# Kernel optimization log

Measured on AMD Instinct MI355X. Metric: run time of the kernel, lower is better.

The kernel has to match this reference:

```python
import jax, jax.numpy as jnp
import numpy as np

N_NODES = 50000
N_EDGES = 800000
NODE_DIM = 128
HIDDEN = 128
N_LAYERS = 2
EPS = 1e-5


def _layer_norm(h, gamma, beta):
    mu = jnp.mean(h, axis=-1, keepdims=True)
    var = jnp.mean(jnp.square(h - mu), axis=-1, keepdims=True)
    return (h - mu) * jax.lax.rsqrt(var + EPS) * gamma + beta


def setup_inputs() -> dict:
    key = jax.random.key(0)
    ks = jax.random.split(key, 12)
    s = 0.05  # small init scale for numerical sanity
    x = jax.random.normal(ks[0], (N_NODES, NODE_DIM), jnp.float32)
    edge_index = jax.random.randint(ks[1], (2, N_EDGES), 0, N_NODES, dtype=jnp.int64)
    # node_encoder: Linear(node_dim -> hidden)
    W_enc = jax.random.normal(ks[2], (HIDDEN, NODE_DIM), jnp.float32) * s
    b_enc = jnp.zeros((HIDDEN,), jnp.float32)
    # per-layer params, stacked over layers (L leading dim)
    Wm1 = jax.random.normal(ks[3], (N_LAYERS, HIDDEN, 2 * HIDDEN), jnp.float32) * s
    bm1 = jnp.zeros((N_LAYERS, HIDDEN), jnp.float32)
    Wm2 = jax.random.normal(ks[4], (N_LAYERS, HIDDEN, HIDDEN), jnp.float32) * s
    bm2 = jnp.zeros((N_LAYERS, HIDDEN), jnp.float32)
    Wu = jax.random.normal(ks[5], (N_LAYERS, HIDDEN, 2 * HIDDEN), jnp.float32) * s
    bu = jnp.zeros((N_LAYERS, HIDDEN), jnp.float32)
    gamma = jnp.ones((N_LAYERS, HIDDEN), jnp.float32)
    beta = jnp.zeros((N_LAYERS, HIDDEN), jnp.float32)
    # output_proj: Linear(hidden -> hidden)
    W_out = jax.random.normal(ks[6], (HIDDEN, HIDDEN), jnp.float32) * s
    b_out = jnp.zeros((HIDDEN,), jnp.float32)
    return {
        "x": x, "edge_index": edge_index,
        "W_enc": W_enc, "b_enc": b_enc,
        "Wm1": Wm1, "bm1": bm1, "Wm2": Wm2, "bm2": bm2,
        "Wu": Wu, "bu": bu, "gamma": gamma, "beta": beta,
        "W_out": W_out, "b_out": b_out,
    }


def reference(x, edge_index, W_enc, b_enc, Wm1, bm1, Wm2, bm2, Wu, bu, gamma, beta, W_out, b_out):
    row, col = edge_index[0], edge_index[1]
    h = x @ W_enc.T + b_enc  # [N, H]
    for l in range(N_LAYERS):
        # gather -> concat -> message MLP  ([E, 2H] -> [E, H])
        m = jnp.concatenate([h[row], h[col]], axis=-1)
        m = jax.nn.relu(m @ Wm1[l].T + bm1[l])
        m = m @ Wm2[l].T + bm2[l]
        # scatter_add over destination nodes (col)
        agg = jax.ops.segment_sum(m, col, num_segments=N_NODES)  # [N, H]
        upd = jnp.concatenate([h, agg], axis=-1) @ Wu[l].T + bu[l]
        h = _layer_norm(h + upd, gamma[l], beta[l])
    return h @ W_out.T + b_out  # node_embeddings [N, H]
```

## Files before the change

kernel.cpp:

```cpp
#include <hip/hip_runtime.h>

#define N_NODES 50000
#define N_EDGES 800000
#define HID 128
#define EPS 1e-5f
#define NBKT 782
#define ESLICE 3125
#define NSLICE 256

typedef __attribute__((ext_vector_type(8))) short s16x8;
typedef __attribute__((ext_vector_type(4))) float f32x4;
typedef __attribute__((ext_vector_type(4))) int i32x4;

__device__ __forceinline__ unsigned short f2bf(float f) {
  unsigned int u = __float_as_uint(f);
  u += 0x7fffu + ((u >> 16) & 1u);
  return (unsigned short)(u >> 16);
}
__device__ __forceinline__ unsigned int pack2(float a, float b) {
  return (unsigned int)f2bf(a) | ((unsigned int)f2bf(b) << 16);
}
__device__ __forceinline__ float bflo(unsigned int u) { return __uint_as_float(u << 16); }
__device__ __forceinline__ float bfhi(unsigned int u) { return __uint_as_float(u & 0xffff0000u); }
__device__ __forceinline__ float bf2f(unsigned short u) { return __uint_as_float((unsigned int)u << 16); }

__global__ __launch_bounds__(256) void prep_hist_kernel(
    const float* __restrict__ W_enc, const float* __restrict__ W_out,
    const float* __restrict__ Wm1, const float* __restrict__ Wu,
    const float* __restrict__ Wm2, const float* __restrict__ bm2,
    unsigned int* __restrict__ Wenc_b, unsigned int* __restrict__ Wout_b,
    unsigned int* __restrict__ Wpq_b, unsigned short* __restrict__ Wcat_b,
    float* __restrict__ bfold, const int* __restrict__ ei, int* __restrict__ bcounts) {
  __shared__ int lhist[NBKT];
  const int b = blockIdx.x, t = threadIdx.x;
  if (b >= 449) {
    const int e0 = (b - 449) * ESLICE;
    for (int i = t; i < NBKT; i += 256) lhist[i] = 0;
    __syncthreads();
    for (int e = e0 + t; e < e0 + ESLICE; e += 256)
      atomicAdd(&lhist[ei[N_EDGES + e] >> 6], 1);
    __syncthreads();
    for (int i = t; i < NBKT; i += 256)
      if (lhist[i]) atomicAdd(&bcounts[i], lhist[i]);
    return;
  }
  if (b < 32) {
    int i = b * 256 + t;
    Wenc_b[i] = pack2(W_enc[2 * i], W_enc[2 * i + 1]);
  } else if (b < 64) {
    int i = (b - 32) * 256 + t;
    Wout_b[i] = pack2(W_out[2 * i], W_out[2 * i + 1]);
  } else if (b < 192) {
    int i = (b - 64) * 256 + t;
    int k2 = i & 63;
    int c = (i >> 6) & 255;
    int l = i >> 14;
    const float* srow = Wm1 + ((size_t)l * 128 + (c & 127)) * 256 + ((c >> 7) << 7);
    Wpq_b[i] = pack2(srow[2 * k2], srow[2 * k2 + 1]);
  } else if (b < 448) {
    int i = (b - 192) * 256 + t;
    int k = i & 255, c = (i >> 8) & 127, l = i >> 15;
    const float* wrow = Wu + ((size_t)l * 128 + c) * 256;
    float v;
    if (k < 128) {
      v = wrow[k];
    } else {
      const float* wb = wrow + 128;
      const float* m2 = Wm2 + (size_t)l * 128 * 128 + (k - 128);
      float s = 0.f;
      for (int j = 0; j < 128; ++j) s += wb[j] * m2[(size_t)j * 128];
      v = s;
    }
    Wcat_b[i] = f2bf(v);
  } else {
    int l = t >> 7, c = t & 127;
    const float* wb = Wu + ((size_t)l * 128 + c) * 256 + 128;
    const float* bv = bm2 + l * 128;
    float s = 0.f;
    for (int j = 0; j < 128; ++j) s += wb[j] * bv[j];
    bfold[t] = s;
  }
}

__global__ __launch_bounds__(1024) void bscan_kernel(const int* __restrict__ bcounts,
                                                     int* __restrict__ boff,
                                                     int* __restrict__ bcursor) {
  __shared__ int wtot[16];
  const int t = threadIdx.x, lane = t & 63, w = t >> 6;
  int v = (t < NBKT) ? bcounts[t] : 0;
  int s = v;
#pragma unroll
  for (int off = 1; off < 64; off <<= 1) {
    int tt = __shfl_up(s, off);
    if (lane >= off) s += tt;
  }
  if (lane == 63) wtot[w] = s;
  __syncthreads();
  int woff = 0;
#pragma unroll
  for (int j = 0; j < 16; ++j) { int tv = wtot[j]; if (j < w) woff += tv; }
  int excl = woff + (s - v);
  if (t < NBKT) { boff[t] = excl; bcursor[t] = excl; }
  if (t == NBKT) boff[NBKT] = excl;
}

__global__ __launch_bounds__(256) void bscatter_kernel(const int* __restrict__ ei,
                                                       int* __restrict__ bcursor,
                                                       unsigned int* __restrict__ ebuf) {
  __shared__ int lhist[784];
  __shared__ int lstart[784];
  __shared__ int lcur[784];
  __shared__ int gbase[784];
  __shared__ unsigned int staged[ESLICE];
  __shared__ int wtot[4];
  const int t = threadIdx.x, lane = t & 63, w = t >> 6;
  const int e0 = blockIdx.x * ESLICE;

  for (int i = t; i < 784; i += 256) lhist[i] = 0;
  __syncthreads();
  for (int e = e0 + t; e < e0 + ESLICE; e += 256)
    atomicAdd(&lhist[ei[N_EDGES + e] >> 6], 1);
  __syncthreads();

  int tsum = 0;
  if (t < 196) tsum = lhist[4 * t] + lhist[4 * t + 1] + lhist[4 * t + 2] + lhist[4 * t + 3];
  int inc = tsum;
#pragma unroll
  for (int off = 1; off < 64; off <<= 1) {
    int tt = __shfl_up(inc, off);
    if (lane >= off) inc += tt;
  }
  if (lane == 63) wtot[w] = inc;
  __syncthreads();
  int woff = 0;
#pragma unroll
  for (int j = 0; j < 4; ++j) { int tv = wtot[j]; if (j < w) woff += tv; }
  if (t < 196) {
    int run = woff + inc - tsum;
#pragma unroll
    for (int j = 0; j < 4; ++j) {
      lstart[4 * t + j] = run;
      lcur[4 * t + j] = run;
      run += lhist[4 * t + j];
    }
  }
  for (int bk = t; bk < NBKT; bk += 256)
    gbase[bk] = lhist[bk] ? atomicAdd(&bcursor[bk], lhist[bk]) : 0;
  __syncthreads();

  for (int e = e0 + t; e < e0 + ESLICE; e += 256) {
    int s = ei[e], d = ei[N_EDGES + e];
    int pos = atomicAdd(&lcur[d >> 6], 1);
    staged[pos] = (unsigned int)s | ((unsigned int)(d & 63) << 16) |
                  ((unsigned int)(d >> 6) << 22);
  }
  __syncthreads();

  for (int i = t; i < ESLICE; i += 256) {
    unsigned int pk = staged[i];
    int bk = pk >> 22;
    ebuf[gbase[bk] + (i - lstart[bk])] = pk;
  }
}

__global__ __launch_bounds__(256) void sort64_kernel(const unsigned int* __restrict__ ebuf,
                                                     const int* __restrict__ boff,
                                                     unsigned int* __restrict__ esrc,
                                                     int* __restrict__ noff,
                                                     int* __restrict__ counts) {
  __shared__ int hist[64];
  __shared__ int lcur[64];
  const int b = blockIdx.x, t = threadIdx.x;
  const int e0 = boff[b], e1 = boff[b + 1];
  if (t < 64) hist[t] = 0;
  __syncthreads();
  for (int e = e0 + t; e < e1; e += 256)
    atomicAdd(&hist[(ebuf[e] >> 16) & 63], 1);
  __syncthreads();
  if (t < 64) {
    int v = hist[t];
    int s = v;
#pragma unroll
    for (int off = 1; off < 64; off <<= 1) {
      int tt = __shfl_up(s, off);
      if (t >= off) s += tt;
    }
    lcur[t] = s - v;
    int node = b * 64 + t;
    if (node < N_NODES) {
      noff[node] = e0 + s - v;
      counts[node] = v;
    }
  }
  __syncthreads();
  for (int e = e0 + t; e < e1; e += 256) {
    unsigned int pk = ebuf[e];
    int pos = atomicAdd(&lcur[(pk >> 16) & 63], 1);
    esrc[e0 + pos] = pk & 0xffffu;
  }
  if (b == NBKT - 1 && t == 0) noff[N_NODES] = e1;
}

__global__ __launch_bounds__(256) void aggregate4_kernel(
    const unsigned int* __restrict__ pq32, const float* __restrict__ bm1,
    const int* __restrict__ noff, const unsigned int* __restrict__ esrc,
    unsigned int* __restrict__ rb32) {
  const int node = blockIdx.x * 4 + (threadIdx.x >> 6);
  const int lane = threadIdx.x & 63;
  const int l = lane & 31;
  const int eh = lane >> 5;
  uint2 qv = *(const uint2*)(pq32 + (size_t)node * 128 + 64 + 2 * l);
  float4 bv = *(const float4*)(bm1 + 4 * l);
  float q0 = bflo(qv.x) + bv.x, q1 = bfhi(qv.x) + bv.y;
  float q2 = bflo(qv.y) + bv.z, q3 = bfhi(qv.y) + bv.w;
  float a0 = 0.f, a1 = 0.f, a2 = 0.f, a3 = 0.f;
  const int i0 = noff[node], i1 = noff[node + 1];
  const int nfull = (i1 - i0) >> 3;
  int idx = i0 + eh;
  for (int j = 0; j < nfull; ++j, idx += 8) {
    int s0 = esrc[idx], s1 = esrc[idx + 2], s2 = esrc[idx + 4], s3 = esrc[idx + 6];
    uint2 u0 = *(const uint2*)(pq32 + (size_t)s0 * 128 + 2 * l);
    uint2 u1 = *(const uint2*)(pq32 + (size_t)s1 * 128 + 2 * l);
    uint2 u2 = *(const uint2*)(pq32 + (size_t)s2 * 128 + 2 * l);
    uint2 u3 = *(const uint2*)(pq32 + (size_t)s3 * 128 + 2 * l);
    a0 += fmaxf(bflo(u0.x) + q0, 0.f) + fmaxf(bflo(u1.x) + q0, 0.f) +
          fmaxf(bflo(u2.x) + q0, 0.f) + fmaxf(bflo(u3.x) + q0, 0.f);
    a1 += fmaxf(bfhi(u0.x) + q1, 0.f) + fmaxf(bfhi(u1.x) + q1, 0.f) +
          fmaxf(bfhi(u2.x) + q1, 0.f) + fmaxf(bfhi(u3.x) + q1, 0.f);
    a2 += fmaxf(bflo(u0.y) + q2, 0.f) + fmaxf(bflo(u1.y) + q2, 0.f) +
          fmaxf(bflo(u2.y) + q2, 0.f) + fmaxf(bflo(u3.y) + q2, 0.f);
    a3 += fmaxf(bfhi(u0.y) + q3, 0.f) + fmaxf(bfhi(u1.y) + q3, 0.f) +
          fmaxf(bfhi(u2.y) + q3, 0.f) + fmaxf(bfhi(u3.y) + q3, 0.f);
  }
  for (; idx < i1; idx += 2) {
    uint2 u0 = *(const uint2*)(pq32 + (size_t)esrc[idx] * 128 + 2 * l);
    a0 += fmaxf(bflo(u0.x) + q0, 0.f);
    a1 += fmaxf(bfhi(u0.x) + q1, 0.f);
    a2 += fmaxf(bflo(u0.y) + q2, 0.f);
    a3 += fmaxf(bfhi(u0.y) + q3, 0.f);
  }
  a0 += __shfl_xor(a0, 32);
  a1 += __shfl_xor(a1, 32);
  a2 += __shfl_xor(a2, 32);
  a3 += __shfl_xor(a3, 32);
  if (lane < 32) {
    uint2 r;
    r.x = pack2(a0, a1);
    r.y = pack2(a2, a3);
    *(uint2*)(rb32 + (size_t)node * 64 + 2 * l) = r;
  }
}

template <int KS, bool AF32, bool DUAL, int MODE>
__global__ __launch_bounds__(256, DUAL ? 1 : 2) void gemm3(
    const void* __restrict__ A0v, const unsigned short* __restrict__ A1,
    const unsigned short* __restrict__ W, const float* __restrict__ bias,
    const int* __restrict__ deg, const float* __restrict__ bias2,
    const float* __restrict__ gamma, const float* __restrict__ beta,
    const unsigned short* __restrict__ hres, float* __restrict__ outF,
    unsigned short* __restrict__ outB, int outw) {
  constexpr int KW = KS * 32;
  constexpr int NFRAG = KS * 8;
  __shared__ short Bs[NFRAG * 512];
  const int lane = threadIdx.x & 63;
  const int w = threadIdx.x >> 6;
  const int cl = lane & 15;
  const int kb = (lane >> 4) * 8;
  const int co = blockIdx.y * 128;
  W += (size_t)blockIdx.y * 128 * KW;

  for (int f = w; f < NFRAG; f += 4) {
    int nt = f & 7, ks = f >> 3;
    s16x8 bv = *(const s16x8*)(W + (size_t)(nt * 16 + cl) * KW + ks * 32 + kb);
    *(s16x8*)(Bs + f * 512 + lane * 8) = bv;
  }
  __syncthreads();

  s16x8 breg[KS][8];
#pragma unroll
  for (int ks = 0; ks < KS; ++ks)
#pragma unroll
    for (int nt = 0; nt < 8; ++nt)
      breg[ks][nt] = *(const s16x8*)(Bs + (ks * 8 + nt) * 512 + lane * 8);

  float bs[8], b2[8], gs[8], bes[8];
#pragma unroll
  for (int nt = 0; nt < 8; ++nt) {
    int col = nt * 16 + cl;
    bs[nt] = bias ? bias[col] : 0.f;
    if constexpr (MODE == 2) {
      b2[nt] = bias2[col];
      gs[nt] = gamma[col];
      bes[nt] = beta[col];
    }
  }

  const int step = gridDim.x * 4;
  for (int rt = blockIdx.x * 4 + w; rt < 3125; rt += step) {
    const int arow = rt * 16 + cl;
    f32x4 acc[8];
#pragma unroll
    for (int i = 0; i < 8; ++i) acc[i] = (f32x4){0.f, 0.f, 0.f, 0.f};
#pragma unroll
    for (int ks = 0; ks < KS; ++ks) {
      s16x8 a;
      if constexpr (AF32) {
        const float* ap = (const float*)A0v + (size_t)arow * HID + ks * 32 + kb;
        float4 lo = *(const float4*)ap;
        float4 hi = *(const float4*)(ap + 4);
        i32x4 ai = {(int)pack2(lo.x, lo.y), (int)pack2(lo.z, lo.w),
                    (int)pack2(hi.x, hi.y), (int)pack2(hi.z, hi.w)};
        a = __builtin_bit_cast(s16x8, ai);
      } else if constexpr (DUAL) {
        const unsigned short* base = (ks < KS / 2) ? (const unsigned short*)A0v : A1;
        int kss = (ks < KS / 2) ? ks : ks - KS / 2;
        a = *(const s16x8*)(base + (size_t)arow * HID + kss * 32 + kb);
      } else {
        a = *(const s16x8*)((const unsigned short*)A0v + (size_t)arow * HID + ks * 32 + kb);
      }
#pragma unroll
      for (int nt = 0; nt < 8; ++nt)
        acc[nt] = __builtin_amdgcn_mfma_f32_16x16x32_bf16(a, breg[ks][nt], acc[nt], 0, 0, 0);
    }

    const int rbase = rt * 16 + (lane >> 4) * 4;
    if constexpr (MODE == 2) {
#pragma unroll
      for (int reg = 0; reg < 4; ++reg) {
        int row = rbase + reg;
        float dv = (float)deg[row];
        float v[8];
        float s = 0.f, s2 = 0.f;
#pragma unroll
        for (int nt = 0; nt < 8; ++nt) {
          float hv = bf2f(hres[(size_t)row * HID + nt * 16 + cl]);
          v[nt] = acc[nt][reg] + bs[nt] + dv * b2[nt] + hv;
          s += v[nt];
          s2 += v[nt] * v[nt];
        }
#pragma unroll
        for (int m = 1; m < 16; m <<= 1) {
          s += __shfl_xor(s, m);
          s2 += __shfl_xor(s2, m);
        }
        float mu = s * (1.f / 128.f);
        float var = s2 * (1.f / 128.f) - mu * mu;
        float inv = rsqrtf(var + EPS);
#pragma unroll
        for (int nt = 0; nt < 8; ++nt) {
          float o = (v[nt] - mu) * inv * gs[nt] + bes[nt];
          outB[(size_t)row * HID + nt * 16 + cl] = f2bf(o);
        }
      }
    } else {
#pragma unroll
      for (int reg = 0; reg < 4; ++reg) {
        int row = rbase + reg;
#pragma unroll
        for (int nt = 0; nt < 8; ++nt) {
          float vv = acc[nt][reg] + bs[nt];
          if constexpr (MODE == 0) outF[(size_t)row * outw + co + nt * 16 + cl] = vv;
          else outB[(size_t)row * outw + co + nt * 16 + cl] = f2bf(vv);
        }
      }
    }
  }
}

extern "C" void kernel_launch(void* const* d_in, const int* in_sizes, int n_in,
                              void* d_out, int out_size, void* d_ws, size_t ws_size,
                              hipStream_t stream) {
  const float* x     = (const float*)d_in[0];
  const int*   ei    = (const int*)d_in[1];
  const float* W_enc = (const float*)d_in[2];
  const float* b_enc = (const float*)d_in[3];
  const float* Wm1   = (const float*)d_in[4];
  const float* bm1   = (const float*)d_in[5];
  const float* Wm2   = (const float*)d_in[6];
  const float* bm2   = (const float*)d_in[7];
  const float* Wu    = (const float*)d_in[8];
  const float* bu    = (const float*)d_in[9];
  const float* gamma = (const float*)d_in[10];
  const float* beta  = (const float*)d_in[11];
  const float* W_out = (const float*)d_in[12];
  const float* b_out = (const float*)d_in[13];
  float* out = (float*)d_out;

  char* ws = (char*)d_ws;
  const size_t NBH = (size_t)N_NODES * HID * 2;

  unsigned short* hb = (unsigned short*)(ws);
  unsigned short* pq = (unsigned short*)(ws + NBH);
  unsigned short* rb = (unsigned short*)(ws + 3 * NBH);
  char* wp = ws + 4 * NBH;
  unsigned short* Wenc_b = (unsigned short*)wp;
  unsigned short* Wout_b = Wenc_b + 16384;
  unsigned short* Wpq_b  = Wout_b + 16384;
  unsigned short* Wcat_b = Wpq_b + 65536;
  float*          bfold  = (float*)(Wcat_b + 65536);
  int* counts  = (int*)(bfold + 256);
  int* noff    = counts + N_NODES;
  int* boff    = noff + N_NODES + 1;
  int* bcounts = boff + NBKT + 1;
  int* bcursor = bcounts + NBKT;
  unsigned int* esrc = (unsigned int*)(bcursor + NBKT);
  unsigned int* ebuf = (unsigned int*)(ws + NBH);

  hipMemsetAsync(bcounts, 0, NBKT * sizeof(int), stream);
  prep_hist_kernel<<<449 + NSLICE, 256, 0, stream>>>(
      W_enc, W_out, Wm1, Wu, Wm2, bm2, (unsigned int*)Wenc_b, (unsigned int*)Wout_b,
      (unsigned int*)Wpq_b, Wcat_b, bfold, ei, bcounts);
  bscan_kernel<<<1, 1024, 0, stream>>>(bcounts, boff, bcursor);
  bscatter_kernel<<<NSLICE, 256, 0, stream>>>(ei, bcursor, ebuf);
  sort64_kernel<<<NBKT, 256, 0, stream>>>(ebuf, boff, esrc, noff, counts);

  gemm3<4, true, false, 1><<<512, 256, 0, stream>>>(
      x, nullptr, Wenc_b, b_enc, nullptr, nullptr, nullptr, nullptr, nullptr,
      nullptr, hb, HID);

  for (int l = 0; l < 2; ++l) {
    const unsigned short* Wpql  = Wpq_b + l * 32768;
    const unsigned short* Wcatl = Wcat_b + l * 32768;
    const float* bm1l = bm1 + l * HID;
    const float* bul  = bu + l * HID;
    const float* bfl  = bfold + l * HID;
    const float* gl   = gamma + l * HID;
    const float* bl   = beta + l * HID;

    gemm3<4, false, false, 1><<<dim3(512, 2), 256, 0, stream>>>(
        hb, nullptr, Wpql, nullptr, nullptr, nullptr, nullptr, nullptr, nullptr,
        nullptr, pq, 256);
    aggregate4_kernel<<<12500, 256, 0, stream>>>((const unsigned int*)pq, bm1l, noff,
                                                 esrc, (unsigned int*)rb);
    gemm3<8, false, true, 2><<<256, 256, 0, stream>>>(
        hb, rb, Wcatl, bul, counts, bfl, gl, bl, hb, nullptr, hb, HID);
  }

  gemm3<4, false, false, 0><<<512, 256, 0, stream>>>(
      hb, nullptr, Wout_b, b_out, nullptr, nullptr, nullptr, nullptr, nullptr,
      out, nullptr, HID);
}
```

Before: 222.0 us.

## Merge preprocessing kernels with GEMMs, deterministic histogram, 16-byte aggregation gathers

Each slice now writes its bucket histogram to a per-slice array, and a new column-sum kernel reduces it, which removes the memset and the global atomics. The bucket scatter is merged with the encoder GEMM in one launch, and the per-node sort is merged with the layer-0 PQ GEMM, so independent work shares launches and fills the GPU together. Edge source indices are stored as 16-bit values, and aggregation uses uint4 loads with 16 lanes per node and four edges in flight per lane. The merged kernels take on the launch bounds and shared-memory footprint of their larger half, which may lower occupancy for the sort part.

```diff
diff --git a/kernel.cpp b/kernel.cpp
--- a/kernel.cpp
+++ b/kernel.cpp
@@ -30,18 +30,18 @@
     const float* __restrict__ Wm2, const float* __restrict__ bm2,
     unsigned int* __restrict__ Wenc_b, unsigned int* __restrict__ Wout_b,
     unsigned int* __restrict__ Wpq_b, unsigned short* __restrict__ Wcat_b,
-    float* __restrict__ bfold, const int* __restrict__ ei, int* __restrict__ bcounts) {
+    float* __restrict__ bfold, const int* __restrict__ ei, int* __restrict__ shist) {
   __shared__ int lhist[NBKT];
   const int b = blockIdx.x, t = threadIdx.x;
   if (b >= 449) {
-    const int e0 = (b - 449) * ESLICE;
+    const int sl = b - 449;
+    const int e0 = sl * ESLICE;
     for (int i = t; i < NBKT; i += 256) lhist[i] = 0;
     __syncthreads();
     for (int e = e0 + t; e < e0 + ESLICE; e += 256)
       atomicAdd(&lhist[ei[N_EDGES + e] >> 6], 1);
     __syncthreads();
-    for (int i = t; i < NBKT; i += 256)
-      if (lhist[i]) atomicAdd(&bcounts[i], lhist[i]);
+    for (int i = t; i < NBKT; i += 256) shist[sl * NBKT + i] = lhist[i];
     return;
   }
   if (b < 32) {
@@ -82,6 +82,15 @@
   }
 }
 
+__global__ __launch_bounds__(256) void colsum_kernel(const int* __restrict__ shist,
+                                                     int* __restrict__ bcounts) {
+  int b = blockIdx.x * 256 + threadIdx.x;
+  if (b >= NBKT) return;
+  int s = 0;
+  for (int j = 0; j < NSLICE; ++j) s += shist[j * NBKT + b];
+  bcounts[b] = s;
+}
+
 __global__ __launch_bounds__(1024) void bscan_kernel(const int* __restrict__ bcounts,
                                                      int* __restrict__ boff,
                                                      int* __restrict__ bcursor) {
@@ -104,88 +113,85 @@
   if (t == NBKT) boff[NBKT] = excl;
 }
 
-__global__ __launch_bounds__(256) void bscatter_kernel(const int* __restrict__ ei,
-                                                       int* __restrict__ bcursor,
-                                                       unsigned int* __restrict__ ebuf) {
-  __shared__ int lhist[784];
-  __shared__ int lstart[784];
-  __shared__ int lcur[784];
-  __shared__ int gbase[784];
-  __shared__ unsigned int staged[ESLICE];
-  __shared__ int wtot[4];
+struct BscatSmem {
+  int lhist[784], lstart[784], lcur[784], gbase[784];
+  unsigned int staged[ESLICE];
+  int wtot[4];
+};
+struct Sort64Smem { int hist[64]; int lcur[64]; };
+
+__device__ __forceinline__ void bscatter_dev(BscatSmem& sm, const int* ei, int* bcursor,
+                                             unsigned int* ebuf, int bx) {
   const int t = threadIdx.x, lane = t & 63, w = t >> 6;
-  const int e0 = blockIdx.x * ESLICE;
-
-  for (int i = t; i < 784; i += 256) lhist[i] = 0;
+  const int e0 = bx * ESLICE;
+
+  for (int i = t; i < 784; i += 256) sm.lhist[i] = 0;
   __syncthreads();
   for (int e = e0 + t; e < e0 + ESLICE; e += 256)
-    atomicAdd(&lhist[ei[N_EDGES + e] >> 6], 1);
+    atomicAdd(&sm.lhist[ei[N_EDGES + e] >> 6], 1);
   __syncthreads();
 
   int tsum = 0;
-  if (t < 196) tsum = lhist[4 * t] + lhist[4 * t + 1] + lhist[4 * t + 2] + lhist[4 * t + 3];
+  if (t < 196)
+    tsum = sm.lhist[4 * t] + sm.lhist[4 * t + 1] + sm.lhist[4 * t + 2] + sm.lhist[4 * t + 3];
   int inc = tsum;
 #pragma unroll
   for (int off = 1; off < 64; off <<= 1) {
     int tt = __shfl_up(inc, off);
     if (lane >= off) inc += tt;
   }
-  if (lane == 63) wtot[w] = inc;
+  if (lane == 63) sm.wtot[w] = inc;
   __syncthreads();
   int woff = 0;
 #pragma unroll
-  for (int j = 0; j < 4; ++j) { int tv = wtot[j]; if (j < w) woff += tv; }
+  for (int j = 0; j < 4; ++j) { int tv = sm.wtot[j]; if (j < w) woff += tv; }
   if (t < 196) {
     int run = woff + inc - tsum;
 #pragma unroll
     for (int j = 0; j < 4; ++j) {
-      lstart[4 * t + j] = run;
-      lcur[4 * t + j] = run;
-      run += lhist[4 * t + j];
+      sm.lstart[4 * t + j] = run;
+      sm.lcur[4 * t + j] = run;
+      run += sm.lhist[4 * t + j];
     }
   }
   for (int bk = t; bk < NBKT; bk += 256)
-    gbase[bk] = lhist[bk] ? atomicAdd(&bcursor[bk], lhist[bk]) : 0;
+    sm.gbase[bk] = sm.lhist[bk] ? atomicAdd(&bcursor[bk], sm.lhist[bk]) : 0;
   __syncthreads();
 
   for (int e = e0 + t; e < e0 + ESLICE; e += 256) {
     int s = ei[e], d = ei[N_EDGES + e];
-    int pos = atomicAdd(&lcur[d >> 6], 1);
-    staged[pos] = (unsigned int)s | ((unsigned int)(d & 63) << 16) |
-                  ((unsigned int)(d >> 6) << 22);
+    int pos = atomicAdd(&sm.lcur[d >> 6], 1);
+    sm.staged[pos] = (unsigned int)s | ((unsigned int)(d & 63) << 16) |
+                     ((unsigned int)(d >> 6) << 22);
   }
   __syncthreads();
 
   for (int i = t; i < ESLICE; i += 256) {
-    unsigned int pk = staged[i];
+    unsigned int pk = sm.staged[i];
     int bk = pk >> 22;
-    ebuf[gbase[bk] + (i - lstart[bk])] = pk;
-  }
-}
-
-__global__ __launch_bounds__(256) void sort64_kernel(const unsigned int* __restrict__ ebuf,
-                                                     const int* __restrict__ boff,
-                                                     unsigned int* __restrict__ esrc,
-                                                     int* __restrict__ noff,
-                                                     int* __restrict__ counts) {
-  __shared__ int hist[64];
-  __shared__ int lcur[64];
-  const int b = blockIdx.x, t = threadIdx.x;
+    ebuf[sm.gbase[bk] + (i - sm.lstart[bk])] = pk;
+  }
+}
+
+__device__ __forceinline__ void sort64_dev(Sort64Smem& sm, const unsigned int* ebuf,
+                                           const int* boff, unsigned short* esrc,
+                                           int* noff, int* counts, int b) {
+  const int t = threadIdx.x;
   const int e0 = boff[b], e1 = boff[b + 1];
-  if (t < 64) hist[t] = 0;
+  if (t < 64) sm.hist[t] = 0;
   __syncthreads();
   for (int e = e0 + t; e < e1; e += 256)
-    atomicAdd(&hist[(ebuf[e] >> 16) & 63], 1);
+    atomicAdd(&sm.hist[(ebuf[e] >> 16) & 63], 1);
   __syncthreads();
   if (t < 64) {
-    int v = hist[t];
+    int v = sm.hist[t];
     int s = v;
 #pragma unroll
     for (int off = 1; off < 64; off <<= 1) {
       int tt = __shfl_up(s, off);
       if (t >= off) s += tt;
     }
-    lcur[t] = s - v;
+    sm.lcur[t] = s - v;
     int node = b * 64 + t;
     if (node < N_NODES) {
       noff[node] = e0 + s - v;
@@ -195,79 +201,29 @@
   __syncthreads();
   for (int e = e0 + t; e < e1; e += 256) {
     unsigned int pk = ebuf[e];
-    int pos = atomicAdd(&lcur[(pk >> 16) & 63], 1);
-    esrc[e0 + pos] = pk & 0xffffu;
+    int pos = atomicAdd(&sm.lcur[(pk >> 16) & 63], 1);
+    esrc[e0 + pos] = (unsigned short)(pk & 0xffffu);
   }
   if (b == NBKT - 1 && t == 0) noff[N_NODES] = e1;
 }
 
-__global__ __launch_bounds__(256) void aggregate4_kernel(
-    const unsigned int* __restrict__ pq32, const float* __restrict__ bm1,
-    const int* __restrict__ noff, const unsigned int* __restrict__ esrc,
-    unsigned int* __restrict__ rb32) {
-  const int node = blockIdx.x * 4 + (threadIdx.x >> 6);
-  const int lane = threadIdx.x & 63;
-  const int l = lane & 31;
-  const int eh = lane >> 5;
-  uint2 qv = *(const uint2*)(pq32 + (size_t)node * 128 + 64 + 2 * l);
-  float4 bv = *(const float4*)(bm1 + 4 * l);
-  float q0 = bflo(qv.x) + bv.x, q1 = bfhi(qv.x) + bv.y;
-  float q2 = bflo(qv.y) + bv.z, q3 = bfhi(qv.y) + bv.w;
-  float a0 = 0.f, a1 = 0.f, a2 = 0.f, a3 = 0.f;
-  const int i0 = noff[node], i1 = noff[node + 1];
-  const int nfull = (i1 - i0) >> 3;
-  int idx = i0 + eh;
-  for (int j = 0; j < nfull; ++j, idx += 8) {
-    int s0 = esrc[idx], s1 = esrc[idx + 2], s2 = esrc[idx + 4], s3 = esrc[idx + 6];
-    uint2 u0 = *(const uint2*)(pq32 + (size_t)s0 * 128 + 2 * l);
-    uint2 u1 = *(const uint2*)(pq32 + (size_t)s1 * 128 + 2 * l);
-    uint2 u2 = *(const uint2*)(pq32 + (size_t)s2 * 128 + 2 * l);
-    uint2 u3 = *(const uint2*)(pq32 + (size_t)s3 * 128 + 2 * l);
-    a0 += fmaxf(bflo(u0.x) + q0, 0.f) + fmaxf(bflo(u1.x) + q0, 0.f) +
-          fmaxf(bflo(u2.x) + q0, 0.f) + fmaxf(bflo(u3.x) + q0, 0.f);
-    a1 += fmaxf(bfhi(u0.x) + q1, 0.f) + fmaxf(bfhi(u1.x) + q1, 0.f) +
-          fmaxf(bfhi(u2.x) + q1, 0.f) + fmaxf(bfhi(u3.x) + q1, 0.f);
-    a2 += fmaxf(bflo(u0.y) + q2, 0.f) + fmaxf(bflo(u1.y) + q2, 0.f) +
-          fmaxf(bflo(u2.y) + q2, 0.f) + fmaxf(bflo(u3.y) + q2, 0.f);
-    a3 += fmaxf(bfhi(u0.y) + q3, 0.f) + fmaxf(bfhi(u1.y) + q3, 0.f) +
-          fmaxf(bfhi(u2.y) + q3, 0.f) + fmaxf(bfhi(u3.y) + q3, 0.f);
-  }
-  for (; idx < i1; idx += 2) {
-    uint2 u0 = *(const uint2*)(pq32 + (size_t)esrc[idx] * 128 + 2 * l);
-    a0 += fmaxf(bflo(u0.x) + q0, 0.f);
-    a1 += fmaxf(bfhi(u0.x) + q1, 0.f);
-    a2 += fmaxf(bflo(u0.y) + q2, 0.f);
-    a3 += fmaxf(bfhi(u0.y) + q3, 0.f);
-  }
-  a0 += __shfl_xor(a0, 32);
-  a1 += __shfl_xor(a1, 32);
-  a2 += __shfl_xor(a2, 32);
-  a3 += __shfl_xor(a3, 32);
-  if (lane < 32) {
-    uint2 r;
-    r.x = pack2(a0, a1);
-    r.y = pack2(a2, a3);
-    *(uint2*)(rb32 + (size_t)node * 64 + 2 * l) = r;
-  }
-}
-
 template <int KS, bool AF32, bool DUAL, int MODE>
-__global__ __launch_bounds__(256, DUAL ? 1 : 2) void gemm3(
-    const void* __restrict__ A0v, const unsigned short* __restrict__ A1,
-    const unsigned short* __restrict__ W, const float* __restrict__ bias,
-    const int* __restrict__ deg, const float* __restrict__ bias2,
-    const float* __restrict__ gamma, const float* __restrict__ beta,
-    const unsigned short* __restrict__ hres, float* __restrict__ outF,
-    unsigned short* __restrict__ outB, int outw) {
+__device__ __forceinline__ void gemm3_dev(
+    short* Bs, int bx, int gx, int by,
+    const void* A0v, const unsigned short* A1,
+    const unsigned short* W, const float* bias,
+    const int* deg, const float* bias2,
+    const float* gamma, const float* beta,
+    const unsigned short* hres, float* outF,
+    unsigned short* outB, int outw) {
   constexpr int KW = KS * 32;
   constexpr int NFRAG = KS * 8;
-  __shared__ short Bs[NFRAG * 512];
   const int lane = threadIdx.x & 63;
   const int w = threadIdx.x >> 6;
   const int cl = lane & 15;
   const int kb = (lane >> 4) * 8;
-  const int co = blockIdx.y * 128;
-  W += (size_t)blockIdx.y * 128 * KW;
+  const int co = by * 128;
+  W += (size_t)by * 128 * KW;
 
   for (int f = w; f < NFRAG; f += 4) {
     int nt = f & 7, ks = f >> 3;
@@ -295,8 +251,8 @@
     }
   }
 
-  const int step = gridDim.x * 4;
-  for (int rt = blockIdx.x * 4 + w; rt < 3125; rt += step) {
+  const int step = gx * 4;
+  for (int rt = bx * 4 + w; rt < 3125; rt += step) {
     const int arow = rt * 16 + cl;
     f32x4 acc[8];
 #pragma unroll
@@ -364,6 +320,108 @@
         }
       }
     }
+  }
+}
+
+template <int KS, bool AF32, bool DUAL, int MODE>
+__global__ __launch_bounds__(256, DUAL ? 1 : 2) void gemm3(
+    const void* __restrict__ A0v, const unsigned short* __restrict__ A1,
+    const unsigned short* __restrict__ W, const float* __restrict__ bias,
+    const int* __restrict__ deg, const float* __restrict__ bias2,
+    const float* __restrict__ gamma, const float* __restrict__ beta,
+    const unsigned short* __restrict__ hres, float* __restrict__ outF,
+    unsigned short* __restrict__ outB, int outw) {
+  __shared__ short Bs[KS * 8 * 512];
+  gemm3_dev<KS, AF32, DUAL, MODE>(Bs, blockIdx.x, gridDim.x, blockIdx.y, A0v, A1, W, bias,
+                                  deg, bias2, gamma, beta, hres, outF, outB, outw);
+}
+
+union MergedSmem1 { BscatSmem b; short Bs[32 * 512]; };
+__global__ __launch_bounds__(256, 2) void k_bscat_enc(
+    const int* __restrict__ ei, int* __restrict__ bcursor, unsigned int* __restrict__ ebuf,
+    const float* __restrict__ x, const unsigned short* __restrict__ Wenc,
+    const float* __restrict__ b_enc, unsigned short* __restrict__ hb) {
+  __shared__ MergedSmem1 sm;
+  if (blockIdx.x < NSLICE) {
+    bscatter_dev(sm.b, ei, bcursor, ebuf, blockIdx.x);
+  } else {
+    gemm3_dev<4, true, false, 1>(sm.Bs, blockIdx.x - NSLICE, 512, 0, x, nullptr, Wenc, b_enc,
+                                 nullptr, nullptr, nullptr, nullptr, nullptr, nullptr, hb, HID);
+  }
+}
+
+union MergedSmem2 { Sort64Smem s; short Bs[32 * 512]; };
+__global__ __launch_bounds__(256, 2) void k_sort_pq(
+    const unsigned int* __restrict__ ebuf, const int* __restrict__ boff,
+    unsigned short* __restrict__ esrc, int* __restrict__ noff, int* __restrict__ counts,
+    const unsigned short* __restrict__ hb, const unsigned short* __restrict__ Wpq,
+    unsigned short* __restrict__ pq) {
+  __shared__ MergedSmem2 sm;
+  if (blockIdx.x < NBKT) {
+    sort64_dev(sm.s, ebuf, boff, esrc, noff, counts, blockIdx.x);
+  } else {
+    int bb = blockIdx.x - NBKT;
+    gemm3_dev<4, false, false, 1>(sm.Bs, bb & 511, 512, bb >> 9, hb, nullptr, Wpq, nullptr,
+                                  nullptr, nullptr, nullptr, nullptr, nullptr, nullptr, pq, 256);
+  }
+}
+
+__device__ __forceinline__ void acc8(float* acc, const float* qf, uint4 u) {
+  acc[0] += fmaxf(bflo(u.x) + qf[0], 0.f);
+  acc[1] += fmaxf(bfhi(u.x) + qf[1], 0.f);
+  acc[2] += fmaxf(bflo(u.y) + qf[2], 0.f);
+  acc[3] += fmaxf(bfhi(u.y) + qf[3], 0.f);
+  acc[4] += fmaxf(bflo(u.z) + qf[4], 0.f);
+  acc[5] += fmaxf(bfhi(u.z) + qf[5], 0.f);
+  acc[6] += fmaxf(bflo(u.w) + qf[6], 0.f);
+  acc[7] += fmaxf(bfhi(u.w) + qf[7], 0.f);
+}
+
+__global__ __launch_bounds__(256) void aggregate5_kernel(
+    const uint4* __restrict__ pq4, const float* __restrict__ bm1,
+    const int* __restrict__ noff, const unsigned short* __restrict__ esrc,
+    uint4* __restrict__ rb4) {
+  const int node = blockIdx.x * 4 + (threadIdx.x >> 6);
+  const int lane = threadIdx.x & 63;
+  const int l = lane & 15;
+  const int eh = lane >> 4;
+  uint4 qv = pq4[(size_t)node * 32 + 16 + l];
+  float4 b0 = *(const float4*)(bm1 + 8 * l);
+  float4 b1 = *(const float4*)(bm1 + 8 * l + 4);
+  float qf[8] = {bflo(qv.x) + b0.x, bfhi(qv.x) + b0.y, bflo(qv.y) + b0.z, bfhi(qv.y) + b0.w,
+                 bflo(qv.z) + b1.x, bfhi(qv.z) + b1.y, bflo(qv.w) + b1.z, bfhi(qv.w) + b1.w};
+  float acc[8] = {0.f, 0.f, 0.f, 0.f, 0.f, 0.f, 0.f, 0.f};
+  const int i0 = noff[node], i1 = noff[node + 1];
+  const int nfull = (i1 - i0) >> 4;
+  int idx = i0 + eh;
+  for (int j = 0; j < nfull; ++j, idx += 16) {
+    int s0 = esrc[idx], s1 = esrc[idx + 4], s2 = esrc[idx + 8], s3 = esrc[idx + 12];
+    uint4 u0 = pq4[(size_t)s0 * 32 + l];
+    uint4 u1 = pq4[(size_t)s1 * 32 + l];
+    uint4 u2 = pq4[(size_t)s2 * 32 + l];
+    uint4 u3 = pq4[(size_t)s3 * 32 + l];
+    acc8(acc, qf, u0);
+    acc8(acc, qf, u1);
+    acc8(acc, qf, u2);
+    acc8(acc, qf, u3);
+  }
+  while (idx < i1) {
+    uint4 u = pq4[(size_t)esrc[idx] * 32 + l];
+    acc8(acc, qf, u);
+    idx += 4;
+  }
+#pragma unroll
+  for (int j = 0; j < 8; ++j) {
+    acc[j] += __shfl_xor(acc[j], 16);
+    acc[j] += __shfl_xor(acc[j], 32);
+  }
+  if (lane < 16) {
+    uint4 r;
+    r.x = pack2(acc[0], acc[1]);
+    r.y = pack2(acc[2], acc[3]);
+    r.z = pack2(acc[4], acc[5]);
+    r.w = pack2(acc[6], acc[7]);
+    rb4[(size_t)node * 16 + l] = r;
   }
 }
 
@@ -403,23 +461,19 @@
   int* boff    = noff + N_NODES + 1;
   int* bcounts = boff + NBKT + 1;
   int* bcursor = bcounts + NBKT;
-  unsigned int* esrc = (unsigned int*)(bcursor + NBKT);
-  unsigned int* ebuf = (unsigned int*)(ws + NBH);
-
-  hipMemsetAsync(bcounts, 0, NBKT * sizeof(int), stream);
+  unsigned short* esrc = (unsigned short*)(bcursor + NBKT);
+  unsigned int* ebuf = (unsigned int*)(esrc + N_EDGES);
+  int* shist = (int*)(ebuf + N_EDGES);
+
   prep_hist_kernel<<<449 + NSLICE, 256, 0, stream>>>(
       W_enc, W_out, Wm1, Wu, Wm2, bm2, (unsigned int*)Wenc_b, (unsigned int*)Wout_b,
-      (unsigned int*)Wpq_b, Wcat_b, bfold, ei, bcounts);
+      (unsigned int*)Wpq_b, Wcat_b, bfold, ei, shist);
+  colsum_kernel<<<4, 256, 0, stream>>>(shist, bcounts);
   bscan_kernel<<<1, 1024, 0, stream>>>(bcounts, boff, bcursor);
-  bscatter_kernel<<<NSLICE, 256, 0, stream>>>(ei, bcursor, ebuf);
-  sort64_kernel<<<NBKT, 256, 0, stream>>>(ebuf, boff, esrc, noff, counts);
-
-  gemm3<4, true, false, 1><<<512, 256, 0, stream>>>(
-      x, nullptr, Wenc_b, b_enc, nullptr, nullptr, nullptr, nullptr, nullptr,
-      nullptr, hb, HID);
+  k_bscat_enc<<<NSLICE + 512, 256, 0, stream>>>(ei, bcursor, ebuf, x, Wenc_b, b_enc, hb);
+  k_sort_pq<<<NBKT + 1024, 256, 0, stream>>>(ebuf, boff, esrc, noff, counts, hb, Wpq_b, pq);
 
   for (int l = 0; l < 2; ++l) {
-    const unsigned short* Wpql  = Wpq_b + l * 32768;
     const unsigned short* Wcatl = Wcat_b + l * 32768;
     const float* bm1l = bm1 + l * HID;
     const float* bul  = bu + l * HID;
@@ -427,13 +481,14 @@
     const float* gl   = gamma + l * HID;
     const float* bl   = beta + l * HID;
 
-    gemm3<4, false, false, 1><<<dim3(512, 2), 256, 0, stream>>>(
-        hb, nullptr, Wpql, nullptr, nullptr, nullptr, nullptr, nullptr, nullptr,
-        nullptr, pq, 256);
-    aggregate4_kernel<<<12500, 256, 0, stream>>>((const unsigned int*)pq, bm1l, noff,
-                                                 esrc, (unsigned int*)rb);
+    aggregate5_kernel<<<12500, 256, 0, stream>>>((const uint4*)pq, bm1l, noff, esrc,
+                                                 (uint4*)rb);
     gemm3<8, false, true, 2><<<256, 256, 0, stream>>>(
         hb, rb, Wcatl, bul, counts, bfl, gl, bl, hb, nullptr, hb, HID);
+    if (l == 0)
+      gemm3<4, false, false, 1><<<dim3(512, 2), 256, 0, stream>>>(
+          hb, nullptr, Wpq_b + 32768, nullptr, nullptr, nullptr, nullptr, nullptr, nullptr,
+          nullptr, pq, 256);
   }
 
   gemm3<4, false, false, 0><<<512, 256, 0, stream>>>(
```

New measurement: 205.3 us. 7.5% less time.
